# Kernel optimization log

Measured on AMD Instinct MI355X. Metric: run time of the kernel, lower is better.

## Reference

```python
import jax, jax.numpy as jnp
import numpy as np


def _quantum_act(x, act_w):
    # LearnedQuantumActivation, eval mode (no phase noise): softmax-weighted mix of 9 activations
    w = jax.nn.softmax(act_w)
    mish = x * jnp.tanh(jax.nn.softplus(x))
    return (w[0] * jax.nn.sigmoid(x) + w[1] * jax.nn.elu(x) + w[2] * jnp.tanh(x)
            + w[3] * jax.nn.relu(x) + w[4] * jax.nn.silu(x)
            + w[5] * jax.nn.gelu(x, approximate=False) + w[6] * jax.nn.selu(x)
            + w[7] * mish + w[8] * x)


def setup_inputs() -> dict:
    B, D, U, N = 1024, 1024, 2048, 4      # batch, input_dim, max_units, num_branches
    M, MD, O, H = 2048, 1024, 512, 64     # memory_size, memory_dim, output_dim, critic hidden
    key = jax.random.key(0)
    ks = jax.random.split(key, 16)
    g = lambda k, shape, s=0.02: jax.random.normal(k, shape, dtype=jnp.float32) * s
    return {
        "x": jax.random.normal(ks[0], (B, D), dtype=jnp.float32),
        "w": g(ks[1], (D, U, N)),
        "b": jnp.zeros((U, N), jnp.float32),
        "gate_w": g(ks[2], (D, N)), "gate_b": jnp.zeros((N,), jnp.float32),
        "act_w": jnp.ones((9,), jnp.float32),
        "mask": jnp.ones((U,), jnp.float32),          # neuron_mask, initial_units == max_units
        "mem": g(ks[3], (M, MD), 0.05),
        "att_w": g(ks[4], (U, M)), "att_b": jnp.zeros((M,), jnp.float32),
        "write_w": g(ks[5], (U, MD)), "write_b": jnp.zeros((MD,), jnp.float32),
        "update_gate": jnp.full((M,), 0.5, jnp.float32),
        "out_w": g(ks[6], (U, O)), "out_b": jnp.zeros((O,), jnp.float32),
        "cw1": g(ks[7], (MD, H // 2)), "cb1": jnp.zeros((H // 2,), jnp.float32),
        "cw2": g(ks[8], (O, H // 2)), "cb2": jnp.zeros((H // 2,), jnp.float32),
        "cw3": g(ks[9], (U, H // 2)), "cb3": jnp.zeros((H // 2,), jnp.float32),
        "cw4": g(ks[10], (3 * (H // 2), H)), "cb4": jnp.zeros((H,), jnp.float32),
        "cw5": g(ks[11], (H, 2)), "cb5": jnp.zeros((2,), jnp.float32),
        "meta_threshold": jnp.float32(0.5),
    }


def reference(x, w, b, gate_w, gate_b, act_w, mask, mem, att_w, att_b,
              write_w, write_b, update_gate, out_w, out_b,
              cw1, cb1, cw2, cb2, cw3, cb3, cw4, cb4, cw5, cb5, meta_threshold):
    # Dendritic plastic dense: per-branch projections mixed by a learned softmax branch gate
    pre = jnp.einsum('bi,iun->bun', x, w) + b               # (B, U, N)
    gate = jax.nn.softmax(x @ gate_w + gate_b, axis=-1)     # (B, N)
    hidden = _quantum_act(jnp.einsum('bun,bn->bu', pre, gate), act_w) * mask  # (B, U)
    # Episodic memory read + write (write is returned instead of in-place assign)
    read_att = jax.nn.softmax(hidden @ att_w + att_b, axis=-1)  # (B, M)
    read = read_att @ mem                                       # (B, MD)
    cand = jnp.tanh(hidden @ write_w + write_b)                 # (B, MD)
    u = (jnp.mean(read_att, axis=0) * update_gate)[:, None]     # (M, 1)
    new_mem = mem * (1.0 - u) + u * jnp.mean(cand, axis=0)      # (M, MD)
    # Prediction head
    preds = hidden @ out_w + out_b                              # (B, O)
    # Metacognitive critic gating
    mf = jax.nn.relu(read @ cw1 + cb1)
    pf = jax.nn.relu(preds @ cw2 + cb2)
    hf = jax.nn.relu(hidden @ cw3 + cb3)
    fused = jax.nn.relu(jnp.concatenate([mf, pf, hf], axis=-1) @ cw4 + cb4)
    outs = fused @ cw5 + cb5
    gating = jax.nn.sigmoid(outs[:, 0:1] - meta_threshold)
    return (preds * gating, new_mem)
```

## Files before the change

### kernel.cpp

```cpp
#include <hip/hip_runtime.h>
#include <hip/hip_bf16.h>
#include <math.h>

typedef __attribute__((ext_vector_type(4))) float f32x4;
typedef __attribute__((ext_vector_type(8))) short s16x8;
typedef __attribute__((ext_vector_type(4))) short s16x4;
typedef __hip_bfloat16 bf16;

#define MB (1024ull*1024ull)
#define GATE_OFF    (0ull)
#define ACTW_OFF    (16ull*1024)
#define U_OFF       (20ull*1024)
#define CMEAN_OFF   (28ull*1024)
#define PART_OFF    (64ull*1024)
#define HIDDEN_OFF  (1ull*MB)
#define RATT_OFF    (5ull*MB)
#define CAND_OFF    (9ull*MB)
#define PREDS_OFF   (11ull*MB)
#define READ_OFF    (13ull*MB)
#define XBF_OFF     (17ull*MB)
#define WT_OFF      (19ull*MB)
#define CATT_OFF    (35ull*MB)
#define MEMT_OFF    (49ull*MB)
#define READ2_OFF   WT_OFF

__device__ __forceinline__ short f2bf_s(float f) {
    bf16 h = __float2bfloat16(f);
    return *reinterpret_cast<short*>(&h);
}

__device__ __forceinline__ void async_load16(const bf16* g, short* l) {
    __builtin_amdgcn_global_load_lds((const __attribute__((address_space(1))) void*)g,
                                     (__attribute__((address_space(3))) void*)l, 16, 0, 0);
}

__device__ __forceinline__ float fast_tanh(float x) {
    float e2x = __expf(2.f * x);
    return 1.f - 2.f / (e2x + 1.f);
}

__device__ __forceinline__ float qact(float x, const float* w) {
    float ex  = __expf(x);
    float r1  = 1.f / (1.f + ex);
    float sig = 1.f - r1;
    float em1 = ex - 1.f;
    float elu = x > 0.f ? x : em1;
    float e2x = ex * ex;
    float th  = 1.f - 2.f / (e2x + 1.f);
    float rel = fmaxf(x, 0.f);
    float silu = x * sig;
    float u   = 0.7978845608028654f * (x + 0.044715f * x * x * x);
    float e2u = __expf(2.f * u);
    float gel = x * (1.f - 1.f / (e2u + 1.f));
    float sel = 1.0507009873554805f * (x > 0.f ? x : 1.6732632423543772f * em1);
    float t   = 1.f + ex;
    float t2  = t * t;
    float mish = x * (1.f - 2.f / (t2 + 1.f));
    return w[0]*sig + w[1]*elu + w[2]*th + w[3]*rel + w[4]*silu
         + w[5]*gel + w[6]*sel + w[7]*mish + w[8]*x;
}

__device__ __forceinline__ void do_transpose(const float* __restrict__ in,
                                             bf16* __restrict__ out, int R, int C,
                                             int bx, int by, int t, short* tile) {
    int k0 = by*64, n0 = bx*64;
    int tx = t & 63, ty = t >> 6;
    #pragma unroll
    for (int j = 0; j < 16; j++) {
        int k = ty + j*4;
        tile[tx*66 + k] = f2bf_s(in[(size_t)(k0 + k)*C + n0 + tx]);
    }
    __syncthreads();
    int kp = t & 31, nrow = t >> 5;
    #pragma unroll
    for (int jj = 0; jj < 8; jj++) {
        int n = nrow + jj*8;
        unsigned lo = (unsigned short)tile[n*66 + kp*2];
        unsigned hi = (unsigned short)tile[n*66 + kp*2 + 1];
        *reinterpret_cast<unsigned*>(&out[(size_t)(n0 + n)*R + k0 + kp*2]) = lo | (hi << 16);
    }
}

__global__ __launch_bounds__(256) void k_prepass(
        const float* __restrict__ x, bf16* __restrict__ xbf,
        const float* __restrict__ gw, const float* __restrict__ gb,
        const float* __restrict__ aw_in,
        float* __restrict__ gate, float* __restrict__ actw,
        const float* __restrict__ w_, bf16* __restrict__ wT) {
    __shared__ short tile[64*66];
    int blk = blockIdx.x, t = threadIdx.x;
    if (blk < 1024) {
        int i = blk*256 + t;
        f32x4 v = ((const f32x4*)x)[i];
        s16x4 o;
        #pragma unroll
        for (int j = 0; j < 4; j++) o[j] = f2bf_s(v[j]);
        ((s16x4*)xbf)[i] = o;
        if (blk == 0 && t == 64) {
            float a[9]; float m = -1e30f;
            for (int i2 = 0; i2 < 9; i2++) { a[i2] = aw_in[i2]; m = fmaxf(m, a[i2]); }
            float ss = 0.f;
            for (int i2 = 0; i2 < 9; i2++) { a[i2] = __expf(a[i2]-m); ss += a[i2]; }
            float inv = 1.f / ss;
            for (int i2 = 0; i2 < 9; i2++) actw[i2] = a[i2]*inv;
        }
    } else if (blk < 2048) {
        int b = blk - 1024, w = t >> 6, lane = t & 63;
        __shared__ float l[4];
        float s = 0.f;
        for (int k = lane; k < 1024; k += 64)
            s += x[(size_t)b*1024 + k] * gw[k*4 + w];
        #pragma unroll
        for (int off = 32; off; off >>= 1) s += __shfl_xor(s, off);
        if (lane == 0) l[w] = s + gb[w];
        __syncthreads();
        if (t == 0) {
            float m = fmaxf(fmaxf(l[0], l[1]), fmaxf(l[2], l[3]));
            float e0 = __expf(l[0]-m), e1 = __expf(l[1]-m), e2 = __expf(l[2]-m), e3 = __expf(l[3]-m);
            float inv = 1.f / (e0+e1+e2+e3);
            gate[b*4+0] = e0*inv; gate[b*4+1] = e1*inv;
            gate[b*4+2] = e2*inv; gate[b*4+3] = e3*inv;
        }
    } else {
        int rel = blk - 2048;
        do_transpose(w_, wT, 1024, 8192, rel & 127, rel >> 7, t, tile);
    }
}

template <int TM>
union SMemT {
    struct { short a[3][TM*32]; short b[3][128*32]; } tl;
    float z[TM*32];
    short tr[64*66];
};

template <int MODE, int TM>
__device__ __forceinline__ void gemm_core(
        int bx, int by, int bz, SMemT<TM>& sm,
        const bf16* __restrict__ A, const bf16* __restrict__ Bt,
        int K, int lda, int ldb, int kOffset,
        const float* __restrict__ bias, const float* __restrict__ bias2,
        const float* __restrict__ bias3,
        float* __restrict__ outF, float* __restrict__ outF2,
        bf16* __restrict__ outH, bf16* __restrict__ outH2,
        const float* __restrict__ gate, const float* __restrict__ actw,
        const float* __restrict__ mask, int outStride) {
    constexpr int MI = TM / 32;
    int t = threadIdx.x, lane = t & 63;
    int rowBase = by * TM, colBase = bx * 128;
    int lm = lane & 15, lq = lane >> 4;
    int w = t >> 6;
    int qm = (w >> 1) * (TM/2), qn = (w & 1) * 64;

    A  += (size_t)kOffset * bz;
    Bt += (size_t)kOffset * bz;

    f32x4 acc[MI][4];
    #pragma unroll
    for (int i = 0; i < MI; i++)
        #pragma unroll
        for (int j = 0; j < 4; j++) acc[i][j] = (f32x4){0.f, 0.f, 0.f, 0.f};

    int cb0 = w*128 + lane, cb1 = cb0 + 64;
    int rb0 = cb0 >> 2, kb0 = ((cb0 & 3) ^ ((rb0 >> 1) & 3)) * 8;
    int rb1 = cb1 >> 2, kb1 = ((cb1 & 3) ^ ((rb1 >> 1) & 3)) * 8;
    int ca0 = (TM == 128) ? (w*128 + lane) : (w*64 + lane);
    int ra0 = ca0 >> 2, ka0 = ((ca0 & 3) ^ ((ra0 >> 1) & 3)) * 8;
    int ca1 = ca0 + 64;
    int ra1 = ca1 >> 2, ka1 = ((ca1 & 3) ^ ((ra1 >> 1) & 3)) * 8;

    auto issueLoads = [&](int k0, int ib) {
        short* bA = sm.tl.a[ib];
        short* bB = sm.tl.b[ib];
        async_load16(A + (size_t)(rowBase + ra0)*lda + k0 + ka0,
                     bA + ((TM == 128) ? w*1024 : w*512));
        if (TM == 128)
            async_load16(A + (size_t)(rowBase + ra1)*lda + k0 + ka1, bA + w*1024 + 512);
        async_load16(Bt + (size_t)(colBase + rb0)*ldb + k0 + kb0, bB + w*1024);
        async_load16(Bt + (size_t)(colBase + rb1)*ldb + k0 + kb1, bB + w*1024 + 512);
    };

    issueLoads(0, 0);
    if (32 < K) issueLoads(32, 1);
    int ib = 0;
    for (int k0 = 0; k0 < K; k0 += 32) {
        if (k0 + 32 < K) {
            if (TM == 128) asm volatile("s_waitcnt vmcnt(4)" ::: "memory");
            else           asm volatile("s_waitcnt vmcnt(3)" ::: "memory");
        } else {
            asm volatile("s_waitcnt vmcnt(0)" ::: "memory");
        }
        __builtin_amdgcn_sched_barrier(0);
        __builtin_amdgcn_s_barrier();
        __builtin_amdgcn_sched_barrier(0);
        int ibn = ib + 2; if (ibn >= 3) ibn -= 3;
        if (k0 + 64 < K) issueLoads(k0 + 64, ibn);
        const short* cA = sm.tl.a[ib];
        const short* cB = sm.tl.b[ib];
        s16x8 af[MI], bfr[4];
        #pragma unroll
        for (int mi = 0; mi < MI; mi++) {
            int r = qm + mi*16 + lm;
            af[mi] = *reinterpret_cast<const s16x8*>(cA + r*32 + ((lq ^ ((r >> 1) & 3)) * 8));
        }
        #pragma unroll
        for (int ni = 0; ni < 4; ni++) {
            int r = qn + ni*16 + lm;
            bfr[ni] = *reinterpret_cast<const s16x8*>(cB + r*32 + ((lq ^ ((r >> 1) & 3)) * 8));
        }
        #pragma unroll
        for (int mi = 0; mi < MI; mi++)
            #pragma unroll
            for (int ni = 0; ni < 4; ni++)
                acc[mi][ni] = __builtin_amdgcn_mfma_f32_16x16x32_bf16(af[mi], bfr[ni], acc[mi][ni], 0, 0, 0);
        ib += 1; if (ib >= 3) ib = 0;
    }

    if (MODE == 4) {
        __syncthreads();
        #pragma unroll
        for (int mi = 0; mi < MI; mi++) {
            int rowl0 = qm + mi*16 + lq*4;
            #pragma unroll
            for (int ni = 0; ni < 4; ni++) {
                int col = colBase + qn + ni*16 + lm;
                int n = col & 3;
                float bb = bias[col];
                f32x4 v = acc[mi][ni];
                #pragma unroll
                for (int r = 0; r < 4; r++) v[r] = (v[r] + bb) * gate[(rowBase + rowl0 + r)*4 + n];
                #pragma unroll
                for (int r = 0; r < 4; r++) v[r] += __shfl_xor(v[r], 1);
                #pragma unroll
                for (int r = 0; r < 4; r++) v[r] += __shfl_xor(v[r], 2);
                if ((lane & 3) == 0) {
                    int ul = ((w & 1) << 4) + ni*4 + (lm >> 2);
                    #pragma unroll
                    for (int r = 0; r < 4; r++)
                        sm.z[(rowl0 + r)*32 + ul] = v[r];
                }
            }
        }
        __syncthreads();
        float aw[9];
        #pragma unroll
        for (int i = 0; i < 9; i++) aw[i] = actw[i];
        int u0 = colBase >> 2;
        #pragma unroll
        for (int i = 0; i < TM/8; i++) {
            int idx = t + i*256;
            int row = idx >> 5, ul = idx & 31;
            int ug = u0 + ul;
            float zz = sm.z[idx];
            outH[(size_t)(rowBase + row)*outStride + ug] = __float2bfloat16(qact(zz, aw) * mask[ug]);
        }
    } else if (MODE == 5) {
        #pragma unroll
        for (int mi = 0; mi < MI; mi++) {
            int row0 = rowBase + qm + mi*16 + lq*4;
            #pragma unroll
            for (int ni = 0; ni < 4; ni++) {
                int col = colBase + qn + ni*16 + lm;
                if (col < 2048) {
                    float bb = bias[col];
                    #pragma unroll
                    for (int r = 0; r < 4; r++)
                        outH[(size_t)(row0 + r)*2048 + col] = __float2bfloat16(acc[mi][ni][r] + bb);
                } else if (col < 3072) {
                    int c = col - 2048;
                    float bb = bias2[c];
                    #pragma unroll
                    for (int r = 0; r < 4; r++)
                        outH2[(size_t)(row0 + r)*1024 + c] = __float2bfloat16(fast_tanh(acc[mi][ni][r] + bb));
                } else {
                    int c = col - 3072;
                    float bb = bias3[c];
                    #pragma unroll
                    for (int r = 0; r < 4; r++)
                        outF[(size_t)(row0 + r)*512 + c] = acc[mi][ni][r] + bb;
                }
            }
        }
    } else {
        float* of = bz ? (outF2 + (size_t)(bz - 1) * 1048576) : outF;
        #pragma unroll
        for (int mi = 0; mi < MI; mi++) {
            int row0 = rowBase + qm + mi*16 + lq*4;
            #pragma unroll
            for (int ni = 0; ni < 4; ni++) {
                int col = colBase + qn + ni*16 + lm;
                #pragma unroll
                for (int r = 0; r < 4; r++)
                    of[(size_t)(row0 + r)*outStride + col] = acc[mi][ni][r];
            }
        }
    }
}

template <int MODE, int TM>
__global__ __launch_bounds__(256, 2) void gemm_bt(
        const bf16* __restrict__ A, const bf16* __restrict__ Bt,
        int K, int lda, int ldb, int kOffset,
        const float* __restrict__ bias, const float* __restrict__ bias2,
        const float* __restrict__ bias3,
        float* __restrict__ outF, float* __restrict__ outF2,
        bf16* __restrict__ outH, bf16* __restrict__ outH2,
        const float* __restrict__ gate, const float* __restrict__ actw,
        const float* __restrict__ mask, int outStride) {
    __shared__ __align__(16) SMemT<TM> sm;
    gemm_core<MODE, TM>(blockIdx.x, blockIdx.y, blockIdx.z, sm,
                        A, Bt, K, lda, ldb, kOffset, bias, bias2, bias3,
                        outF, outF2, outH, outH2, gate, actw, mask, outStride);
}

__global__ __launch_bounds__(256, 2) void k_g1x(
        const bf16* __restrict__ xbf, const bf16* __restrict__ wT,
        const float* __restrict__ bias, bf16* __restrict__ hidden,
        const float* __restrict__ gate, const float* __restrict__ actw,
        const float* __restrict__ mask,
        const float* __restrict__ att_w, const float* __restrict__ write_w,
        const float* __restrict__ out_w, bf16* __restrict__ catT,
        const float* __restrict__ mem, bf16* __restrict__ memT) {
    __shared__ __align__(16) SMemT<128> sm;
    int bid = blockIdx.x, t = threadIdx.x;
    if (bid < 512) {
        gemm_core<4, 128>(bid & 63, bid >> 6, 0, sm, xbf, wT, 1024, 1024, 1024, 0,
                          bias, nullptr, nullptr, nullptr, nullptr, hidden, nullptr,
                          gate, actw, mask, 2048);
    } else {
        int rel = bid - 512;
        if (rel < 1024) {
            do_transpose(att_w, catT, 2048, 2048, rel & 31, rel >> 5, t, sm.tr);
        } else if (rel < 1536) {
            rel -= 1024;
            do_transpose(write_w, catT + 2048ull*2048, 2048, 1024, rel & 15, rel >> 4, t, sm.tr);
        } else if (rel < 1792) {
            rel -= 1536;
            do_transpose(out_w, catT + 3072ull*2048, 2048, 512, rel & 7, rel >> 3, t, sm.tr);
        } else {
            rel -= 1792;
            do_transpose(mem, memT, 2048, 1024, rel & 15, rel >> 4, t, sm.tr);
        }
    }
}

__global__ __launch_bounds__(256) void k_softmax(bf16* __restrict__ ratt) {
    int b = blockIdx.x, t = threadIdx.x, w = t >> 6, lane = t & 63;
    __shared__ float red[8];
    bf16* row = ratt + (size_t)b*2048;
    float v[8];
    float mx = -1e30f;
    #pragma unroll
    for (int j = 0; j < 8; j++) {
        v[j] = __bfloat162float(row[t + j*256]);
        mx = fmaxf(mx, v[j]);
    }
    #pragma unroll
    for (int off = 32; off; off >>= 1) mx = fmaxf(mx, __shfl_xor(mx, off));
    if (lane == 0) red[w] = mx;
    __syncthreads();
    mx = fmaxf(fmaxf(red[0], red[1]), fmaxf(red[2], red[3]));
    float s = 0.f;
    #pragma unroll
    for (int j = 0; j < 8; j++) { v[j] = __expf(v[j] - mx); s += v[j]; }
    #pragma unroll
    for (int off = 32; off; off >>= 1) s += __shfl_xor(s, off);
    if (lane == 0) red[4 + w] = s;
    __syncthreads();
    float inv = 1.f / (red[4] + red[5] + red[6] + red[7]);
    #pragma unroll
    for (int j = 0; j < 8; j++)
        row[t + j*256] = __float2bfloat16(v[j] * inv);
}

__global__ __launch_bounds__(256, 2) void k_g5x(
        const bf16* __restrict__ ratt, const bf16* __restrict__ memT,
        const bf16* __restrict__ cand,
        float* __restrict__ readv, float* __restrict__ readv2,
        float* __restrict__ part) {
    __shared__ __align__(16) SMemT<64> sm;
    int bid = blockIdx.x, t = threadIdx.x;
    if (bid < 512) {
        int bx = bid & 7, by = (bid >> 3) & 15, bz = bid >> 7;
        gemm_core<3, 64>(bx, by, bz, sm, ratt, memT, 512, 2048, 2048, 512,
                         nullptr, nullptr, nullptr, readv, readv2, nullptr, nullptr,
                         nullptr, nullptr, nullptr, 1024);
    } else {
        int rel = bid - 512;
        int ct = rel % 12, rc = rel / 12;
        int col = ct*256 + t;
        const bf16* src; int stride, c;
        if (ct < 8) { src = ratt; stride = 2048; c = col; }
        else        { src = cand; stride = 1024; c = col - 2048; }
        float s = 0.f;
        int r0 = rc*128;
        for (int r2 = 0; r2 < 128; r2++)
            s += __bfloat162float(src[(size_t)(r0 + r2)*stride + c]);
        part[rc*3072 + col] = s;
    }
}

__global__ __launch_bounds__(256) void k_colfin(const float* __restrict__ part,
                                                const float* __restrict__ update_gate,
                                                float* __restrict__ u,
                                                float* __restrict__ cmean) {
    int col = blockIdx.x*256 + threadIdx.x;
    float s = 0.f;
    #pragma unroll
    for (int rc = 0; rc < 8; rc++) s += part[rc*3072 + col];
    s *= (1.f/1024.f);
    if (col < 2048) u[col] = s * update_gate[col];
    else            cmean[col - 2048] = s;
}

__global__ __launch_bounds__(256) void k_fin(
        const float* __restrict__ readv, const float* __restrict__ readv2,
        const float* __restrict__ preds, const bf16* __restrict__ hidden,
        const float* cw1, const float* cb1, const float* cw2, const float* cb2,
        const float* cw3, const float* cb3, const float* cw4, const float* cb4,
        const float* cw5, const float* cb5, const float* thr,
        float* __restrict__ out0,
        const float* __restrict__ mem, const float* __restrict__ u,
        const float* __restrict__ cmean, float* __restrict__ out1) {
    __shared__ __align__(16) float sx[2*1024];
    __shared__ __align__(16) float sp[2*512];
    __shared__ __align__(16) short sh[2*2048];
    __shared__ __align__(16) f32x4 part[2][32][8];
    __shared__ float feat[2][96];
    __shared__ float fused[2][64];
    __shared__ float gsh[2];
    int bid = blockIdx.x, t = threadIdx.x;
    if (bid >= 512) {
        int idx = (bid - 512)*256 + t;
        int m = idx >> 8, d4 = idx & 255;
        float um = u[m];
        f32x4 m4 = ((const f32x4*)mem)[idx];
        f32x4 c4 = ((const f32x4*)cmean)[d4];
        f32x4 o;
        #pragma unroll
        for (int j = 0; j < 4; j++) o[j] = m4[j] * (1.f - um) + um * c4[j];
        ((f32x4*)out1)[idx] = o;
        return;
    }
    int b0 = bid * 2;
    int j4 = t & 7, kg = t >> 3;

    {
        const f32x4* r0 = (const f32x4*)(readv  + (size_t)b0*1024);
        const f32x4* r1 = (const f32x4*)(readv2 + (size_t)b0*1024);
        const f32x4* r2 = (const f32x4*)(readv2 + 1048576 + (size_t)b0*1024);
        const f32x4* r3 = (const f32x4*)(readv2 + 2097152 + (size_t)b0*1024);
        ((f32x4*)sx)[t]       = r0[t] + r1[t] + r2[t] + r3[t];
        ((f32x4*)sx)[t + 256] = r0[t + 256] + r1[t + 256] + r2[t + 256] + r3[t + 256];
    }
    ((f32x4*)sp)[t]       = ((const f32x4*)(preds + (size_t)b0*512))[t];
    ((s16x8*)sh)[t]       = ((const s16x8*)(hidden + (size_t)b0*2048))[t];
    ((s16x8*)sh)[t + 256] = ((const s16x8*)(hidden + (size_t)b0*2048))[t + 256];
    __syncthreads();

    {
        const f32x4* wv = (const f32x4*)cw1;
        f32x4 a0 = (f32x4){0,0,0,0}, a1 = (f32x4){0,0,0,0};
        int k0 = kg*32;
        #pragma unroll 4
        for (int k = k0; k < k0 + 32; k++) {
            f32x4 wq = wv[k*8 + j4];
            a0 += sx[k] * wq;
            a1 += sx[1024 + k] * wq;
        }
        part[0][kg][j4] = a0; part[1][kg][j4] = a1;
    }
    __syncthreads();
    if (t < 64) {
        int r = t >> 5, f = t & 31;
        float s = 0.f;
        #pragma unroll
        for (int i = 0; i < 32; i++) s += part[r][i][f >> 2][f & 3];
        feat[r][f] = fmaxf(s + cb1[f], 0.f);
    }
    __syncthreads();
    {
        const f32x4* wv = (const f32x4*)cw2;
        f32x4 a0 = (f32x4){0,0,0,0}, a1 = (f32x4){0,0,0,0};
        int k0 = kg*16;
        #pragma unroll 4
        for (int k = k0; k < k0 + 16; k++) {
            f32x4 wq = wv[k*8 + j4];
            a0 += sp[k] * wq;
            a1 += sp[512 + k] * wq;
        }
        part[0][kg][j4] = a0; part[1][kg][j4] = a1;
    }
    __syncthreads();
    if (t < 64) {
        int r = t >> 5, f = t & 31;
        float s = 0.f;
        #pragma unroll
        for (int i = 0; i < 32; i++) s += part[r][i][f >> 2][f & 3];
        feat[r][32 + f] = fmaxf(s + cb2[f], 0.f);
    }
    __syncthreads();
    {
        const f32x4* wv = (const f32x4*)cw3;
        f32x4 a0 = (f32x4){0,0,0,0}, a1 = (f32x4){0,0,0,0};
        int k0 = kg*64;
        #pragma unroll 4
        for (int k = k0; k < k0 + 64; k++) {
            f32x4 wq = wv[k*8 + j4];
            float h0 = __bfloat162float(*reinterpret_cast<const bf16*>(&sh[k]));
            float h1 = __bfloat162float(*reinterpret_cast<const bf16*>(&sh[2048 + k]));
            a0 += h0 * wq;
            a1 += h1 * wq;
        }
        part[0][kg][j4] = a0; part[1][kg][j4] = a1;
    }
    __syncthreads();
    if (t < 64) {
        int r = t >> 5, f = t & 31;
        float s = 0.f;
        #pragma unroll
        for (int i = 0; i < 32; i++) s += part[r][i][f >> 2][f & 3];
        feat[r][64 + f] = fmaxf(s + cb3[f], 0.f);
    }
    __syncthreads();
    if (t < 128) {
        int r = t >> 6, uu = t & 63;
        float s = 0.f;
        #pragma unroll 8
        for (int k = 0; k < 96; k++) s += feat[r][k] * cw4[k*64 + uu];
        fused[r][uu] = fmaxf(s + cb4[uu], 0.f);
    }
    __syncthreads();
    if (t < 128) {
        int r = t >> 6, lane = t & 63;
        float v = fused[r][lane] * cw5[lane*2];
        #pragma unroll
        for (int off = 32; off; off >>= 1) v += __shfl_xor(v, off);
        if (lane == 0)
            gsh[r] = 1.f / (1.f + __expf(-(v + cb5[0] - thr[0])));
    }
    __syncthreads();
    #pragma unroll
    for (int idx = t; idx < 1024; idx += 256) {
        int r = idx >> 9, o = idx & 511;
        out0[(size_t)(b0 + r)*512 + o] = sp[r*512 + o] * gsh[r];
    }
}

extern "C" void kernel_launch(void* const* d_in, const int* in_sizes, int n_in,
                              void* d_out, int out_size, void* d_ws, size_t ws_size,
                              hipStream_t stream) {
    const float* x        = (const float*)d_in[0];
    const float* w_       = (const float*)d_in[1];
    const float* b_bias   = (const float*)d_in[2];
    const float* gate_w   = (const float*)d_in[3];
    const float* gate_b   = (const float*)d_in[4];
    const float* act_w    = (const float*)d_in[5];
    const float* mask     = (const float*)d_in[6];
    const float* mem      = (const float*)d_in[7];
    const float* att_w    = (const float*)d_in[8];
    const float* att_b    = (const float*)d_in[9];
    const float* write_w  = (const float*)d_in[10];
    const float* write_b  = (const float*)d_in[11];
    const float* upd_gate = (const float*)d_in[12];
    const float* out_w    = (const float*)d_in[13];
    const float* out_b    = (const float*)d_in[14];
    const float* cw1 = (const float*)d_in[15]; const float* cb1 = (const float*)d_in[16];
    const float* cw2 = (const float*)d_in[17]; const float* cb2 = (const float*)d_in[18];
    const float* cw3 = (const float*)d_in[19]; const float* cb3 = (const float*)d_in[20];
    const float* cw4 = (const float*)d_in[21]; const float* cb4 = (const float*)d_in[22];
    const float* cw5 = (const float*)d_in[23]; const float* cb5 = (const float*)d_in[24];
    const float* thr = (const float*)d_in[25];

    char* ws = (char*)d_ws;
    float* gate   = (float*)(ws + GATE_OFF);
    float* actw   = (float*)(ws + ACTW_OFF);
    float* uvec   = (float*)(ws + U_OFF);
    float* cmean  = (float*)(ws + CMEAN_OFF);
    float* part   = (float*)(ws + PART_OFF);
    bf16*  hidden = (bf16*)(ws + HIDDEN_OFF);
    bf16*  ratt   = (bf16*)(ws + RATT_OFF);
    bf16*  cand   = (bf16*)(ws + CAND_OFF);
    float* preds  = (float*)(ws + PREDS_OFF);
    float* readv  = (float*)(ws + READ_OFF);
    float* readv2 = (float*)(ws + READ2_OFF);
    bf16*  xbf    = (bf16*)(ws + XBF_OFF);
    bf16*  wT     = (bf16*)(ws + WT_OFF);
    bf16*  catT   = (bf16*)(ws + CATT_OFF);
    bf16*  memT   = (bf16*)(ws + MEMT_OFF);

    float* out0 = (float*)d_out;
    float* out1 = out0 + 1024*512;

    k_prepass<<<4096, 256, 0, stream>>>(x, xbf, gate_w, gate_b, act_w, gate, actw, w_, wT);

    k_g1x<<<2816, 256, 0, stream>>>(xbf, wT, b_bias, hidden, gate, actw, mask,
                                    att_w, write_w, out_w, catT, mem, memT);

    gemm_bt<5, 64><<<dim3(28, 16), 256, 0, stream>>>(hidden, catT, 2048, 2048, 2048, 0,
        att_b, write_b, out_b, preds, nullptr, ratt, cand, nullptr, nullptr, nullptr, 0);
    k_softmax<<<1024, 256, 0, stream>>>(ratt);
    k_g5x<<<608, 256, 0, stream>>>(ratt, memT, cand, readv, readv2, part);

    k_colfin<<<12, 256, 0, stream>>>(part, upd_gate, uvec, cmean);
    k_fin<<<2560, 256, 0, stream>>>(readv, readv2, preds, hidden,
        cw1, cb1, cw2, cb2, cw3, cb3, cw4, cb4, cw5, cb5, thr, out0,
        mem, uvec, cmean, out1);
}
```

Before: 259.2 us.

## Move all weight transposes into prepass, drop colfin via atomics, vectorize transpose loads

The att/write/out/mem transposes move out of the first GEMM kernel into the prepass, so the hidden GEMM runs as a plain launch. The column-mean reduction kernel is removed: partial sums are atomically added into u and cmean, which the prepass zeroes. The transpose reads two floats per thread. This cuts one launch and keeps transpose blocks from sharing the GEMM launch, at the cost of a longer prepass, float atomics and run-to-run variation in summation order.

```diff
diff --git a/kernel.cpp b/kernel.cpp
--- a/kernel.cpp
+++ b/kernel.cpp
@@ -3,6 +3,7 @@
 #include <math.h>
 
 typedef __attribute__((ext_vector_type(4))) float f32x4;
+typedef __attribute__((ext_vector_type(2))) float f32x2;
 typedef __attribute__((ext_vector_type(8))) short s16x8;
 typedef __attribute__((ext_vector_type(4))) short s16x4;
 typedef __hip_bfloat16 bf16;
@@ -64,11 +65,13 @@
                                              bf16* __restrict__ out, int R, int C,
                                              int bx, int by, int t, short* tile) {
     int k0 = by*64, n0 = bx*64;
-    int tx = t & 63, ty = t >> 6;
-    #pragma unroll
-    for (int j = 0; j < 16; j++) {
-        int k = ty + j*4;
-        tile[tx*66 + k] = f2bf_s(in[(size_t)(k0 + k)*C + n0 + tx]);
+    int i = t & 31, half = t >> 5;
+    #pragma unroll
+    for (int r = 0; r < 8; r++) {
+        int k = half + r*8;
+        f32x2 v = *reinterpret_cast<const f32x2*>(&in[(size_t)(k0 + k)*C + n0 + i*2]);
+        tile[(i*2 + 0)*66 + k] = f2bf_s(v[0]);
+        tile[(i*2 + 1)*66 + k] = f2bf_s(v[1]);
     }
     __syncthreads();
     int kp = t & 31, nrow = t >> 5;
@@ -86,17 +89,35 @@
         const float* __restrict__ gw, const float* __restrict__ gb,
         const float* __restrict__ aw_in,
         float* __restrict__ gate, float* __restrict__ actw,
-        const float* __restrict__ w_, bf16* __restrict__ wT) {
+        const float* __restrict__ w_, bf16* __restrict__ wT,
+        const float* __restrict__ att_w, const float* __restrict__ write_w,
+        const float* __restrict__ out_w, bf16* __restrict__ catT,
+        const float* __restrict__ mem, bf16* __restrict__ memT,
+        float* __restrict__ zbase) {
     __shared__ short tile[64*66];
     int blk = blockIdx.x, t = threadIdx.x;
-    if (blk < 1024) {
-        int i = blk*256 + t;
+    if (blk < 2048) {
+        do_transpose(w_, wT, 1024, 8192, blk & 127, blk >> 7, t, tile);
+    } else if (blk < 3072) {
+        int rel = blk - 2048;
+        do_transpose(att_w, catT, 2048, 2048, rel & 31, rel >> 5, t, tile);
+    } else if (blk < 3584) {
+        int rel = blk - 3072;
+        do_transpose(write_w, catT + 2048ull*2048, 2048, 1024, rel & 15, rel >> 4, t, tile);
+    } else if (blk < 3840) {
+        int rel = blk - 3584;
+        do_transpose(out_w, catT + 3072ull*2048, 2048, 512, rel & 7, rel >> 3, t, tile);
+    } else if (blk < 4352) {
+        int rel = blk - 3840;
+        do_transpose(mem, memT, 2048, 1024, rel & 15, rel >> 4, t, tile);
+    } else if (blk < 5376) {
+        int i = (blk - 4352)*256 + t;
         f32x4 v = ((const f32x4*)x)[i];
         s16x4 o;
         #pragma unroll
         for (int j = 0; j < 4; j++) o[j] = f2bf_s(v[j]);
         ((s16x4*)xbf)[i] = o;
-        if (blk == 0 && t == 64) {
+        if (blk == 4352 && t == 64) {
             float a[9]; float m = -1e30f;
             for (int i2 = 0; i2 < 9; i2++) { a[i2] = aw_in[i2]; m = fmaxf(m, a[i2]); }
             float ss = 0.f;
@@ -104,8 +125,8 @@
             float inv = 1.f / ss;
             for (int i2 = 0; i2 < 9; i2++) actw[i2] = a[i2]*inv;
         }
-    } else if (blk < 2048) {
-        int b = blk - 1024, w = t >> 6, lane = t & 63;
+    } else if (blk < 6400) {
+        int b = blk - 5376, w = t >> 6, lane = t & 63;
         __shared__ float l[4];
         float s = 0.f;
         for (int k = lane; k < 1024; k += 64)
@@ -122,8 +143,8 @@
             gate[b*4+2] = e2*inv; gate[b*4+3] = e3*inv;
         }
     } else {
-        int rel = blk - 2048;
-        do_transpose(w_, wT, 1024, 8192, rel & 127, rel >> 7, t, tile);
+        int idx = (blk - 6400)*256 + t;
+        ((f32x4*)zbase)[idx] = (f32x4){0.f, 0.f, 0.f, 0.f};
     }
 }
 
@@ -131,7 +152,6 @@
 union SMemT {
     struct { short a[3][TM*32]; short b[3][128*32]; } tl;
     float z[TM*32];
-    short tr[64*66];
 };
 
 template <int MODE, int TM>
@@ -313,37 +333,6 @@
                         outF, outF2, outH, outH2, gate, actw, mask, outStride);
 }
 
-__global__ __launch_bounds__(256, 2) void k_g1x(
-        const bf16* __restrict__ xbf, const bf16* __restrict__ wT,
-        const float* __restrict__ bias, bf16* __restrict__ hidden,
-        const float* __restrict__ gate, const float* __restrict__ actw,
-        const float* __restrict__ mask,
-        const float* __restrict__ att_w, const float* __restrict__ write_w,
-        const float* __restrict__ out_w, bf16* __restrict__ catT,
-        const float* __restrict__ mem, bf16* __restrict__ memT) {
-    __shared__ __align__(16) SMemT<128> sm;
-    int bid = blockIdx.x, t = threadIdx.x;
-    if (bid < 512) {
-        gemm_core<4, 128>(bid & 63, bid >> 6, 0, sm, xbf, wT, 1024, 1024, 1024, 0,
-                          bias, nullptr, nullptr, nullptr, nullptr, hidden, nullptr,
-                          gate, actw, mask, 2048);
-    } else {
-        int rel = bid - 512;
-        if (rel < 1024) {
-            do_transpose(att_w, catT, 2048, 2048, rel & 31, rel >> 5, t, sm.tr);
-        } else if (rel < 1536) {
-            rel -= 1024;
-            do_transpose(write_w, catT + 2048ull*2048, 2048, 1024, rel & 15, rel >> 4, t, sm.tr);
-        } else if (rel < 1792) {
-            rel -= 1536;
-            do_transpose(out_w, catT + 3072ull*2048, 2048, 512, rel & 7, rel >> 3, t, sm.tr);
-        } else {
-            rel -= 1792;
-            do_transpose(mem, memT, 2048, 1024, rel & 15, rel >> 4, t, sm.tr);
-        }
-    }
-}
-
 __global__ __launch_bounds__(256) void k_softmax(bf16* __restrict__ ratt) {
     int b = blockIdx.x, t = threadIdx.x, w = t >> 6, lane = t & 63;
     __shared__ float red[8];
@@ -377,7 +366,8 @@
         const bf16* __restrict__ ratt, const bf16* __restrict__ memT,
         const bf16* __restrict__ cand,
         float* __restrict__ readv, float* __restrict__ readv2,
-        float* __restrict__ part) {
+        const float* __restrict__ update_gate,
+        float* __restrict__ u, float* __restrict__ cmean) {
     __shared__ __align__(16) SMemT<64> sm;
     int bid = blockIdx.x, t = threadIdx.x;
     if (bid < 512) {
@@ -396,21 +386,9 @@
         int r0 = rc*128;
         for (int r2 = 0; r2 < 128; r2++)
             s += __bfloat162float(src[(size_t)(r0 + r2)*stride + c]);
-        part[rc*3072 + col] = s;
-    }
-}
-
-__global__ __launch_bounds__(256) void k_colfin(const float* __restrict__ part,
-                                                const float* __restrict__ update_gate,
-                                                float* __restrict__ u,
-                                                float* __restrict__ cmean) {
-    int col = blockIdx.x*256 + threadIdx.x;
-    float s = 0.f;
-    #pragma unroll
-    for (int rc = 0; rc < 8; rc++) s += part[rc*3072 + col];
-    s *= (1.f/1024.f);
-    if (col < 2048) u[col] = s * update_gate[col];
-    else            cmean[col - 2048] = s;
+        if (ct < 8) atomicAdd(&u[col], s * (update_gate[col] * (1.f/1024.f)));
+        else        atomicAdd(&cmean[col - 2048], s * (1.f/1024.f));
+    }
 }
 
 __global__ __launch_bounds__(256) void k_fin(
@@ -577,7 +555,6 @@
     float* actw   = (float*)(ws + ACTW_OFF);
     float* uvec   = (float*)(ws + U_OFF);
     float* cmean  = (float*)(ws + CMEAN_OFF);
-    float* part   = (float*)(ws + PART_OFF);
     bf16*  hidden = (bf16*)(ws + HIDDEN_OFF);
     bf16*  ratt   = (bf16*)(ws + RATT_OFF);
     bf16*  cand   = (bf16*)(ws + CAND_OFF);
@@ -592,17 +569,18 @@
     float* out0 = (float*)d_out;
     float* out1 = out0 + 1024*512;
 
-    k_prepass<<<4096, 256, 0, stream>>>(x, xbf, gate_w, gate_b, act_w, gate, actw, w_, wT);
-
-    k_g1x<<<2816, 256, 0, stream>>>(xbf, wT, b_bias, hidden, gate, actw, mask,
-                                    att_w, write_w, out_w, catT, mem, memT);
+    k_prepass<<<6403, 256, 0, stream>>>(x, xbf, gate_w, gate_b, act_w, gate, actw,
+                                        w_, wT, att_w, write_w, out_w, catT, mem, memT,
+                                        uvec);
+
+    gemm_bt<4, 128><<<dim3(64, 8), 256, 0, stream>>>(xbf, wT, 1024, 1024, 1024, 0,
+        b_bias, nullptr, nullptr, nullptr, nullptr, hidden, nullptr, gate, actw, mask, 2048);
 
     gemm_bt<5, 64><<<dim3(28, 16), 256, 0, stream>>>(hidden, catT, 2048, 2048, 2048, 0,
         att_b, write_b, out_b, preds, nullptr, ratt, cand, nullptr, nullptr, nullptr, 0);
     k_softmax<<<1024, 256, 0, stream>>>(ratt);
-    k_g5x<<<608, 256, 0, stream>>>(ratt, memT, cand, readv, readv2, part);
-
-    k_colfin<<<12, 256, 0, stream>>>(part, upd_gate, uvec, cmean);
+    k_g5x<<<608, 256, 0, stream>>>(ratt, memT, cand, readv, readv2, upd_gate, uvec, cmean);
+
     k_fin<<<2560, 256, 0, stream>>>(readv, readv2, preds, hidden,
         cw1, cb1, cw2, cb2, cw3, cb3, cw4, cb4, cw5, cb5, thr, out0,
         mem, uvec, cmean, out1);
```

Result: slower. 265.4 us (+2.4%).
